# Kernel optimization log

Measured on AMD Instinct MI355X. Metric: run time of the kernel, lower is better.

Reference implementation:

```python
import jax, jax.numpy as jnp
import numpy as np

N = 131072
BETA = 1.0
E = float(np.e)
BISECT_ITERS = 60  # (v-u)/2^60 << 1e-5 threshold of FIND_MIN


def _smooth_l1(x, beta=BETA):
    d = jnp.abs(x)
    return jnp.where(d < beta, 0.5 * d * d / beta, d - 0.5 * beta)


def _safe_log(w):
    return jnp.log(jnp.maximum(w, 1e-12))


def _eps(w, wp, wh, beta=BETA):
    # epsilon(omega) = smooth_l1((omega-omega_hat)/2) + smooth_l1(log omega - log omega_p)
    return _smooth_l1((w - wh) * 0.5, beta) + _smooth_l1(_safe_log(w) - _safe_log(wp), beta)


def _eps_prime(w, wp, wh, beta=BETA):
    x = (w - wh) * 0.5
    diff = _safe_log(w) - _safe_log(wp)
    return 0.5 * jnp.clip(x / beta, -1.0, 1.0) + jnp.clip(diff / beta, -1.0, 1.0) / jnp.maximum(w, 1e-12)


def _sigma(w, wp, wh, beta=BETA):
    return w * _eps_prime(w, wp, wh, beta)


def _find_min(u, v, f):
    # Vectorized FIND_MIN bisection: fixed-trip bisection + boundary cases.
    u0, v0 = u, v

    def body(_, uv):
        uu, vv = uv
        m = (uu + vv) * 0.5
        c = f(m) >= 0
        return (jnp.where(c, uu, m), jnp.where(c, m, vv))

    uf, vf = jax.lax.fori_loop(0, BISECT_ITERS, body, (u, v))
    m = (uf + vf) * 0.5
    return jnp.where(f(u0) >= 0, u0, jnp.where(f(v0) <= 0, v0, m))


def _solve_o1(wp, wh, a1, b1, beta=BETA):
    w0 = b1 - a1
    fm_e = lambda u, v: _find_min(u, v, lambda w: _eps_prime(w, wp, wh, beta))
    fm_s = lambda u, v: _find_min(u, v, lambda w: _sigma(w, wp, wh, beta))
    branchA = jnp.maximum(w0, wh) < wp
    branchB = jnp.maximum(w0, wp) < wh
    cA = fm_e(jnp.maximum(w0, wh), wp)
    ebeta = float(np.exp(beta))
    # J1..J5 intervals from J_getter
    c2 = fm_e(jnp.maximum(w0, wp), jnp.minimum(float(np.exp(min(beta, 1.0))) * wp, wh))
    c3 = fm_e(jnp.maximum(jnp.maximum(w0, 2.0 * float(np.sqrt(beta))), jnp.maximum(wh - 2.0 * beta, ebeta * wp)), wh)
    base = jnp.maximum(w0, jnp.maximum(wh - 2.0 * beta, E * wp))
    c4 = fm_s(base, jnp.minimum(ebeta, wh))
    disc = jnp.sqrt(jnp.maximum(1.0 - 32.0 / jnp.maximum(wh * wh, 1e-12), 0.0))
    c5 = fm_s(base, jnp.minimum(jnp.minimum(ebeta * wp, wh), wh * 0.25 * (1.0 + disc)))
    c6 = fm_s(jnp.maximum(base, wh * 0.25 * (1.0 - disc)), jnp.minimum(ebeta * wp, wh))
    small = wh <= 4.0 * float(np.sqrt(2.0))
    cands = jnp.stack([w0, wh, c2, c3, c4, c5, c6], axis=-1)  # [N,7]
    evals = _eps(cands, wp[..., None], wh[..., None], beta)
    zeros = jnp.zeros_like(small)
    invalid = jnp.stack([zeros, zeros, zeros, zeros, ~small, small, small], axis=-1)
    evals = jnp.where(invalid, jnp.float32(1e30), evals)
    idx = jnp.argmin(evals, axis=-1)
    wB = jnp.take_along_axis(cands, idx[..., None], axis=-1)[..., 0]
    return jnp.where(branchA, cA, jnp.where(branchB, wB, w0))


def _solve_o2(dp, wp, a2, b2, beta=BETA):
    wh1 = 2.0 * (dp - a2)
    wh2 = 2.0 * (b2 - dp)
    trivial = wp >= jnp.maximum(wh1, wh2)
    w1 = _solve_o1(wp, wh1, a2, b2, beta)
    w2 = _solve_o1(wp, wh2, a2, b2, beta)
    pick1 = _eps(w1, wp, wh1, beta) <= _eps(w2, wp, wh2, beta)
    d = jnp.where(pick1, a2 + 0.5 * w1, b2 + 0.5 * w2)
    w = jnp.where(pick1, w1, w2)
    return jnp.where(trivial, dp, d), jnp.where(trivial, wp, w)


def _case_axis(pred, prop, cases, target, crop, axis):
    if axis == 0:
        lt, rb = cases[:, 0], cases[:, 1]
        d_id, o_id = 0, 2
    else:
        lt, rb = cases[:, 2], cases[:, 3]
        d_id, o_id = 1, 3
    pd, po = pred[:, d_id], pred[:, o_id]
    td, to = target[:, d_id], target[:, o_id]
    ca = 0.5 * (prop[:, d_id] + prop[:, o_id])
    da = prop[:, o_id] - prop[:, d_id]
    # right/bottom cut
    a1r = td - 0.5 * to
    b1r = (crop[:, axis] - ca) / da
    wr = _solve_o1(po, 2.0 * (pd - a1r), a1r, b1r)
    dr = a1r + 0.5 * wr
    # left/top cut
    a1l = -ca / da
    b1l = td + 0.5 * to
    wl = _solve_o1(po, 2.0 * (b1l - pd), a1l, b1l)
    dl = b1l - 0.5 * wl
    # both cut (source passes omega_p=pred[:,d_id] and crop[:,d_id] -- replicated)
    b2 = (crop[:, d_id] - ca) / da
    db, wb = _solve_o2(pd, pd, a1l, b2)
    none_c = (~lt) & (~rb)
    r_c = (~lt) & rb
    l_c = lt & (~rb)
    d_lab = jnp.where(none_c, td, jnp.where(r_c, dr, jnp.where(l_c, dl, db)))
    w_lab = jnp.where(none_c, to, jnp.where(r_c, wr, jnp.where(l_c, wl, wb)))
    return d_lab, w_lab


def setup_inputs() -> dict:
    key = jax.random.key(0)
    k = jax.random.split(key, 8)
    img = jax.random.normal(k[0], (1, 3, 128, 128), jnp.float32)
    pred = jax.random.normal(k[1], (N, 4), jnp.float32) * 0.3
    target = jax.random.normal(k[2], (N, 4), jnp.float32) * 0.3
    xy1 = jax.random.uniform(k[3], (N, 2), jnp.float32) * 800.0
    wh = jax.random.uniform(k[4], (N, 2), jnp.float32) * 180.0 + 20.0
    proposal_list = jnp.stack([xy1[:, 0], xy1[:, 1], xy1[:, 0] + wh[:, 0], xy1[:, 1] + wh[:, 1]], axis=1)
    crop_shapes = jax.random.uniform(k[5], (N, 4), jnp.float32) * 200.0 + 900.0
    cases = jax.random.bernoulli(k[6], 0.5, (N, 4))
    return {"img": img, "pred": pred, "target": target, "crop_shapes": crop_shapes,
            "proposal_list": proposal_list, "cases": cases, "sampling_results": 0}


def reference(img, pred, target, crop_shapes, proposal_list, cases, sampling_results):
    # target/pred dw,dh (cols 2,3) are exponentiated to widths/heights, as in forward
    predw = pred.at[:, 2:4].set(jnp.exp(pred[:, 2:4]))
    targw = target.at[:, 2:4].set(jnp.exp(target[:, 2:4]))
    d0, w0 = _case_axis(predw, proposal_list, cases, targw, crop_shapes, 0)
    d1, w1 = _case_axis(predw, proposal_list, cases, targw, crop_shapes, 1)
    # label layout [dx, dy, w, h] matching label[0..3] of the source
    return jnp.stack([d0, d1, w0, w1], axis=-1)
```

## Files before the change

### kernel.cpp

```cpp
#include <hip/hip_runtime.h>
#include <math.h>

#define BISECT_ITERS 60
#define N_ROWS 131072
#define N_PAIRS (2 * N_ROWS)
#define BLOCK 512
#define NW (BLOCK / 64)

#define E_CONST 2.71828182845904523536f
#define SMALL_THRESH 5.65685424949238019520f
#define LN2F 0.69314718055994530942f
#define LOG1EM12 -27.63102111592854820f

__device__ __forceinline__ float log_cr(float wc) {
    double d = (double)wc;
    long long b = __double_as_longlong(d);
    int e = (int)((b >> 52) & 0x7FF) - 1023;
    double m = __longlong_as_double((b & 0x000FFFFFFFFFFFFFLL) |
                                    0x3FF0000000000000LL);
    if (m > 1.3333333333333333) {
        m *= 0.5;
        e += 1;
    }
    double s = (m - 1.0) / (m + 1.0);
    double s2 = s * s;
    double p = 1.0 / 17.0;
    p = fma(p, s2, 1.0 / 15.0);
    p = fma(p, s2, 1.0 / 13.0);
    p = fma(p, s2, 1.0 / 11.0);
    p = fma(p, s2, 1.0 / 9.0);
    p = fma(p, s2, 1.0 / 7.0);
    p = fma(p, s2, 1.0 / 5.0);
    p = fma(p, s2, 1.0 / 3.0);
    p = fma(p, s2, 1.0);
    double res = fma(2.0 * s, p, (double)e * 0.69314718055994530941723212145818);
    return (float)res;
}

__device__ __forceinline__ float safe_log_f(float w) {
    if (w <= 1e-12f) return LOG1EM12;
    return log_cr(w);
}

__device__ __forceinline__ float clip1f(float x) {
#pragma clang fp contract(off)
    return fminf(fmaxf(x, -1.0f), 1.0f);
}

__device__ __forceinline__ float sl1(float x) {
#pragma clang fp contract(off)
    float d = fabsf(x);
    return (d < 1.0f) ? (0.5f * d) * d : d - 0.5f;
}

__device__ __forceinline__ float eps_f(float w, float wh, float lwp) {
#pragma clang fp contract(off)
    return sl1((w - wh) * 0.5f) + sl1(safe_log_f(w) - lwp);
}

__device__ __forceinline__ float eps_prime_cr(float w, float wh, float lwp) {
#pragma clang fp contract(off)
    float x = (w - wh) * 0.5f;
    float diff = safe_log_f(w) - lwp;
    return 0.5f * clip1f(x) + clip1f(diff) / fmaxf(w, 1e-12f);
}

__device__ __forceinline__ float sigma_cr(float w, float wh, float lwp) {
#pragma clang fp contract(off)
    return w * eps_prime_cr(w, wh, lwp);
}

__device__ __forceinline__ float nlogf(float w) {
    return LN2F * __builtin_amdgcn_logf(fmaxf(w, 1e-12f));
}

__device__ __forceinline__ float epsp_sign(float m, float wh, float lwp) {
    float wm = fmaxf(m, 1e-12f);
    float x = (m - wh) * 0.5f;
    float diff = __builtin_fmaf(LN2F, __builtin_amdgcn_logf(wm), -lwp);
    return __builtin_fmaf(0.5f * clip1f(x), wm, clip1f(diff));
}

__device__ __forceinline__ int fast_epsp_sgn(float x, float wh, float lwp) {
    float wm = fmaxf(x, 1e-12f);
    float F = epsp_sign(x, wh, lwp);
    float tau = 2e-5f * (wm + 1.0f);
    if (F > tau) return 1;
    if (F < -tau) return -1;
    return 0;
}

__device__ __forceinline__ int fast_sigma_sgn(float x, float wh, float lwp) {
    float wm = fmaxf(x, 1e-12f);
    float F = epsp_sign(x, wh, lwp);
    float G = x * F;
    float tau = fabsf(x) * (2e-5f * (wm + 1.0f));
    if (G > tau) return 1;
    if (G < -tau) return -1;
    return 0;
}

__device__ __forceinline__ float fast_eval(float w, float wh, float lwp) {
#pragma clang fp contract(off)
    return sl1((w - wh) * 0.5f) + sl1(nlogf(w) - lwp);
}

__device__ float find_min_e(float u, float v, float wh, float lwp) {
#pragma clang fp contract(off)
    float u0 = u, v0 = v;
#pragma unroll 1
    for (int i = 0; i < BISECT_ITERS; ++i) {
        float m = (u + v) * 0.5f;
        bool frozen = (m == u) || (m == v);
        bool c = epsp_sign(m, wh, lwp) >= 0.0f;
        u = c ? u : m;
        v = c ? m : v;
        if (__all(frozen)) break;
    }
    float m = (u + v) * 0.5f;
    float r = m;
    if (eps_prime_cr(v0, wh, lwp) <= 0.0f) r = v0;
    if (eps_prime_cr(u0, wh, lwp) >= 0.0f) r = u0;
    return r;
}

__device__ __forceinline__ bool ov_e_le(float x, float wh, float lwp) {
    int s = fast_epsp_sgn(x, wh, lwp);
    if (s < 0) return true;
    if (s > 0) return false;
    return eps_prime_cr(x, wh, lwp) <= 0.0f;
}
__device__ __forceinline__ bool ov_e_ge(float x, float wh, float lwp) {
    int s = fast_epsp_sgn(x, wh, lwp);
    if (s > 0) return true;
    if (s < 0) return false;
    return eps_prime_cr(x, wh, lwp) >= 0.0f;
}
__device__ __forceinline__ bool ov_s_le(float x, float wh, float lwp) {
    int s = fast_sigma_sgn(x, wh, lwp);
    if (s < 0) return true;
    if (s > 0) return false;
    return sigma_cr(x, wh, lwp) <= 0.0f;
}
__device__ __forceinline__ bool ov_s_ge(float x, float wh, float lwp) {
    int s = fast_sigma_sgn(x, wh, lwp);
    if (s > 0) return true;
    if (s < 0) return false;
    return sigma_cr(x, wh, lwp) >= 0.0f;
}

__device__ __forceinline__ float argmin7(const float* cands, const float* Ef,
                                         const bool* valid, float wh, float lwp) {
#pragma clang fp contract(off)
    int j = 0;
    float best = Ef[0];
#pragma unroll
    for (int k = 1; k < 7; ++k) {
        if (Ef[k] < best) { best = Ef[k]; j = k; }
    }
    bool need_cr = false;
#pragma unroll
    for (int k = 0; k < 7; ++k) {
        if (k == j) continue;
        float dl = 2e-5f + 2e-6f * (fabsf(best) + fabsf(Ef[k]));
        if (Ef[k] < best + dl &&
            fabsf(cands[k] - cands[j]) > 1e-4f * (1.0f + fabsf(cands[j])))
            need_cr = true;
    }
    if (need_cr) {
        float Ec[7];
#pragma unroll
        for (int k = 0; k < 7; ++k)
            Ec[k] = valid[k] ? eps_f(cands[k], wh, lwp) : 1e30f;
        j = 0;
        best = Ec[0];
#pragma unroll
        for (int k = 1; k < 7; ++k) {
            if (Ec[k] < best) { best = Ec[k]; j = k; }
        }
    }
    return cands[j];
}

struct PairP {
    float pd, po, td, to, a1r, b1r, a1l, b1l;
    int lt, rb;
};

__device__ __forceinline__ PairP load_pair(const float* __restrict__ pred,
                                           const float* __restrict__ target,
                                           const float* __restrict__ crop,
                                           const float* __restrict__ prop,
                                           const int* __restrict__ cases,
                                           int pair) {
#pragma clang fp contract(off)
    int row = pair >> 1, axis = pair & 1;
    int d_id = axis, o_id = axis + 2, r4 = row * 4;
    PairP P;
    P.pd = pred[r4 + d_id];
    P.po = (float)exp((double)pred[r4 + o_id]);
    P.td = target[r4 + d_id];
    P.to = (float)exp((double)target[r4 + o_id]);
    float p_d = prop[r4 + d_id];
    float p_o = prop[r4 + o_id];
    float ca = 0.5f * (p_d + p_o);
    float da = p_o - p_d;
    float crop_a = crop[r4 + axis];
    P.a1r = P.td - 0.5f * P.to;
    P.b1r = (crop_a - ca) / da;
    P.a1l = (-ca) / da;
    P.b1l = P.td + 0.5f * P.to;
    P.lt = cases[r4 + 2 * axis];
    P.rb = cases[r4 + 2 * axis + 1];
    return P;
}

__device__ float solve_B_large(float wp, float wh, float w0, float lwp) {
#pragma clang fp contract(off)
    float ewp = E_CONST * wp;
    float base = fmaxf(w0, fmaxf(wh - 2.0f, ewp));
    float disc = sqrtf(fmaxf(1.0f - 32.0f / fmaxf(wh * wh, 1e-12f), 0.0f));

    float u2 = fmaxf(w0, wp), v2 = fminf(ewp, wh);
    float u3 = fmaxf(fmaxf(w0, 2.0f), fmaxf(wh - 2.0f, ewp)), v3 = wh;
    float u5 = base, v5 = fminf(fminf(ewp, wh), (wh * 0.25f) * (1.0f + disc));
    float u6 = fmaxf(base, (wh * 0.25f) * (1.0f - disc)), v6 = fminf(ewp, wh);
    float u02 = u2, v02 = v2, u03 = u3, v03 = v3;
    float u05 = u5, v05 = v5, u06 = u6, v06 = v6;

#pragma unroll 1
    for (int i = 0; i < BISECT_ITERS; ++i) {
        float m2 = (u2 + v2) * 0.5f;
        float m3 = (u3 + v3) * 0.5f;
        float m5 = (u5 + v5) * 0.5f;
        float m6 = (u6 + v6) * 0.5f;
        bool fr = (m2 == u2 || m2 == v2) && (m3 == u3 || m3 == v3) &&
                  (m5 == u5 || m5 == v5) && (m6 == u6 || m6 == v6);
        bool c2 = epsp_sign(m2, wh, lwp) >= 0.0f;
        bool c3 = epsp_sign(m3, wh, lwp) >= 0.0f;
        bool c5 = (m5 * epsp_sign(m5, wh, lwp)) >= 0.0f;
        bool c6 = (m6 * epsp_sign(m6, wh, lwp)) >= 0.0f;
        u2 = c2 ? u2 : m2; v2 = c2 ? m2 : v2;
        u3 = c3 ? u3 : m3; v3 = c3 ? m3 : v3;
        u5 = c5 ? u5 : m5; v5 = c5 ? m5 : v5;
        u6 = c6 ? u6 : m6; v6 = c6 ? m6 : v6;
        if (__all(fr)) break;
    }

    float c2r = (u2 + v2) * 0.5f;
    if (ov_e_le(v02, wh, lwp)) c2r = v02;
    if (ov_e_ge(u02, wh, lwp)) c2r = u02;
    float c3r = (u3 + v3) * 0.5f;
    if (ov_e_le(v03, wh, lwp)) c3r = v03;
    if (ov_e_ge(u03, wh, lwp)) c3r = u03;
    float c5r = (u5 + v5) * 0.5f;
    if (ov_s_le(v05, wh, lwp)) c5r = v05;
    if (ov_s_ge(u05, wh, lwp)) c5r = u05;
    float c6r = (u6 + v6) * 0.5f;
    if (ov_s_le(v06, wh, lwp)) c6r = v06;
    if (ov_s_ge(u06, wh, lwp)) c6r = u06;

    float cands[7] = {w0, wh, c2r, c3r, 0.0f, c5r, c6r};
    bool valid[7] = {true, true, true, true, false, true, true};
    float Ef[7];
    Ef[0] = fast_eval(w0, wh, lwp);
    Ef[1] = fast_eval(wh, wh, lwp);
    Ef[2] = fast_eval(c2r, wh, lwp);
    Ef[3] = fast_eval(c3r, wh, lwp);
    Ef[4] = 1e30f;
    Ef[5] = fast_eval(c5r, wh, lwp);
    Ef[6] = fast_eval(c6r, wh, lwp);
    return argmin7(cands, Ef, valid, wh, lwp);
}

__device__ float solve_B_small(float wp, float wh, float w0, float lwp) {
#pragma clang fp contract(off)
    float ewp = E_CONST * wp;
    float base = fmaxf(w0, fmaxf(wh - 2.0f, ewp));

    float u2 = fmaxf(w0, wp), v2 = fminf(ewp, wh);
    float u3 = fmaxf(fmaxf(w0, 2.0f), fmaxf(wh - 2.0f, ewp)), v3 = wh;
    float u4 = base, v4 = fminf(E_CONST, wh);
    float u02 = u2, v02 = v2, u03 = u3, v03 = v3, u04 = u4, v04 = v4;

#pragma unroll 1
    for (int i = 0; i < BISECT_ITERS; ++i) {
        float m2 = (u2 + v2) * 0.5f;
        float m3 = (u3 + v3) * 0.5f;
        float m4 = (u4 + v4) * 0.5f;
        bool fr = (m2 == u2 || m2 == v2) && (m3 == u3 || m3 == v3) &&
                  (m4 == u4 || m4 == v4);
        bool c2 = epsp_sign(m2, wh, lwp) >= 0.0f;
        bool c3 = epsp_sign(m3, wh, lwp) >= 0.0f;
        bool c4 = (m4 * epsp_sign(m4, wh, lwp)) >= 0.0f;
        u2 = c2 ? u2 : m2; v2 = c2 ? m2 : v2;
        u3 = c3 ? u3 : m3; v3 = c3 ? m3 : v3;
        u4 = c4 ? u4 : m4; v4 = c4 ? m4 : v4;
        if (__all(fr)) break;
    }

    float c2r = (u2 + v2) * 0.5f;
    if (ov_e_le(v02, wh, lwp)) c2r = v02;
    if (ov_e_ge(u02, wh, lwp)) c2r = u02;
    float c3r = (u3 + v3) * 0.5f;
    if (ov_e_le(v03, wh, lwp)) c3r = v03;
    if (ov_e_ge(u03, wh, lwp)) c3r = u03;
    float c4r = (u4 + v4) * 0.5f;
    if (ov_s_le(v04, wh, lwp)) c4r = v04;
    if (ov_s_ge(u04, wh, lwp)) c4r = u04;

    float cands[7] = {w0, wh, c2r, c3r, c4r, 0.0f, 0.0f};
    bool valid[7] = {true, true, true, true, true, false, false};
    float Ef[7];
    Ef[0] = fast_eval(w0, wh, lwp);
    Ef[1] = fast_eval(wh, wh, lwp);
    Ef[2] = fast_eval(c2r, wh, lwp);
    Ef[3] = fast_eval(c3r, wh, lwp);
    Ef[4] = fast_eval(c4r, wh, lwp);
    Ef[5] = 1e30f;
    Ef[6] = 1e30f;
    return argmin7(cands, Ef, valid, wh, lwp);
}

__global__ __launch_bounds__(BLOCK)
void cabb_fused_kernel(const float* __restrict__ pred,
                       const float* __restrict__ target,
                       const float* __restrict__ crop,
                       const float* __restrict__ prop,
                       const int* __restrict__ cases,
                       float* __restrict__ out) {
#pragma clang fp contract(off)
    __shared__ float qb_wp[2 * BLOCK], qb_wh[2 * BLOCK], qb_w0[2 * BLOCK];
    __shared__ unsigned short qb_code[2 * BLOCK];
    __shared__ float qa_wp[BLOCK], qa_wh[BLOCK], qa_w0[BLOCK];
    __shared__ unsigned short qa_code[BLOCK];
    __shared__ float s_res[2 * BLOCK];
    __shared__ int s_cnt[NW][3];
    __shared__ int s_tot[3];

    int tid = threadIdx.x;
    int wid = tid >> 6;
    int lane = tid & 63;
    unsigned long long lower = (1ULL << lane) - 1ULL;
    int pair = blockIdx.x * BLOCK + tid;

    if (tid < 3) s_tot[tid] = 0;

    PairP P = load_pair(pred, target, crop, prop, cases, pair);

    bool need_b = P.lt && P.rb;
    bool need_l = P.lt && !P.rb;
    bool need_r = !P.lt && P.rb;

    int it_type[2] = {-1, -1};
    float it_wp[2], it_wh[2], it_w0[2];
    unsigned short it_code[2];
    int nit = 0;

    if (need_r || need_l) {
        float wp = P.po;
        float wh = need_l ? 2.0f * (P.b1l - P.pd) : 2.0f * (P.pd - P.a1r);
        float w0 = need_l ? (P.b1l - P.a1l) : (P.b1r - P.a1r);
        bool bA = fmaxf(w0, wh) < wp;
        bool bB = fmaxf(w0, wp) < wh;
        if (bA || bB) {
            it_type[0] = bA ? 2 : (wh <= SMALL_THRESH ? 1 : 0);
            it_wp[0] = wp; it_wh[0] = wh; it_w0[0] = w0;
            it_code[0] = (unsigned short)(tid * 2);
            nit = 1;
        }
    } else if (need_b) {
        float wh1 = 2.0f * (P.pd - P.a1l);
        float wh2 = 2.0f * (P.b1r - P.pd);
        bool trivial = P.pd >= fmaxf(wh1, wh2);
        if (!trivial) {
            float w0 = P.b1r - P.a1l;
            for (int s = 0; s < 2; ++s) {
                float wh = s ? wh2 : wh1;
                bool bA = fmaxf(w0, wh) < P.pd;
                bool bB = fmaxf(w0, P.pd) < wh;
                if (bA || bB) {
                    it_type[nit] = bA ? 2 : (wh <= SMALL_THRESH ? 1 : 0);
                    it_wp[nit] = P.pd; it_wh[nit] = wh; it_w0[nit] = w0;
                    it_code[nit] = (unsigned short)(tid * 2 + s);
                    ++nit;
                }
            }
        }
    }

    for (int k = 0; k < 2; ++k) {
        bool is0 = it_type[k] == 0, is1 = it_type[k] == 1, is2 = it_type[k] == 2;
        unsigned long long m0 = __ballot(is0);
        unsigned long long m1 = __ballot(is1);
        unsigned long long m2 = __ballot(is2);
        if (lane == 0) {
            s_cnt[wid][0] = __popcll(m0);
            s_cnt[wid][1] = __popcll(m1);
            s_cnt[wid][2] = __popcll(m2);
        }
        __syncthreads();
        if (it_type[k] >= 0) {
            int t = it_type[k];
            int base = s_tot[t];
            for (int w = 0; w < wid; ++w) base += s_cnt[w][t];
            unsigned long long mm = t == 0 ? m0 : (t == 1 ? m1 : m2);
            int pos = base + __popcll(mm & lower);
            if (t == 0) {
                qb_wp[pos] = it_wp[k]; qb_wh[pos] = it_wh[k];
                qb_w0[pos] = it_w0[k]; qb_code[pos] = it_code[k];
            } else if (t == 1) {
                int p2 = (2 * BLOCK - 1) - pos;
                qb_wp[p2] = it_wp[k]; qb_wh[p2] = it_wh[k];
                qb_w0[p2] = it_w0[k]; qb_code[p2] = it_code[k];
            } else {
                qa_wp[pos] = it_wp[k]; qa_wh[pos] = it_wh[k];
                qa_w0[pos] = it_w0[k]; qa_code[pos] = it_code[k];
            }
        }
        __syncthreads();
        if (tid < 3) {
            int s = 0;
            for (int w = 0; w < NW; ++w) s += s_cnt[w][tid];
            s_tot[tid] += s;
        }
        __syncthreads();
    }

    int nBl = s_tot[0], nBs = s_tot[1], nA = s_tot[2];

    int nBlC = (nBl + 63) >> 6;
    int nBsC = (nBs + 63) >> 6;
    int nAC = (nA + 63) >> 6;
    int totC = nBlC + nBsC + nAC;
    for (int c = wid; c < totC; c += NW) {
        if (c < nBlC) {
            int i = (c << 6) + lane;
            if (i < nBl) {
                float wp = qb_wp[i], wh = qb_wh[i], w0 = qb_w0[i];
                float lwp = safe_log_f(wp);
                s_res[qb_code[i]] = solve_B_large(wp, wh, w0, lwp);
            }
        } else if (c < nBlC + nBsC) {
            int i = ((c - nBlC) << 6) + lane;
            if (i < nBs) {
                int idx = (2 * BLOCK - 1) - i;
                float wp = qb_wp[idx], wh = qb_wh[idx], w0 = qb_w0[idx];
                float lwp = safe_log_f(wp);
                s_res[qb_code[idx]] = solve_B_small(wp, wh, w0, lwp);
            }
        } else {
            int i = ((c - nBlC - nBsC) << 6) + lane;
            if (i < nA) {
                float wp = qa_wp[i], wh = qa_wh[i], w0 = qa_w0[i];
                float lwp = safe_log_f(wp);
                s_res[qa_code[i]] = find_min_e(fmaxf(w0, wh), wp, wh, lwp);
            }
        }
    }
    __syncthreads();

    int row = pair >> 1, axis = pair & 1;
    int r4 = row * 4;
    float d_lab, w_lab;
    if (need_b) {
        float wh1 = 2.0f * (P.pd - P.a1l);
        float wh2 = 2.0f * (P.b1r - P.pd);
        bool trivial = P.pd >= fmaxf(wh1, wh2);
        if (trivial) {
            d_lab = P.pd;
            w_lab = P.pd;
        } else {
            float w0 = P.b1r - P.a1l;
            bool q1 = (fmaxf(w0, wh1) < P.pd) || (fmaxf(w0, P.pd) < wh1);
            bool q2 = (fmaxf(w0, wh2) < P.pd) || (fmaxf(w0, P.pd) < wh2);
            float s1 = q1 ? s_res[tid * 2] : w0;
            float s2 = q2 ? s_res[tid * 2 + 1] : w0;
            float lwpf = nlogf(P.pd);
            float F1 = sl1((s1 - wh1) * 0.5f) + sl1(nlogf(s1) - lwpf);
            float F2 = sl1((s2 - wh2) * 0.5f) + sl1(nlogf(s2) - lwpf);
            float dl = 3e-5f + 2e-6f * (fabsf(F1) + fabsf(F2));
            bool pick1;
            if (F1 <= F2 - dl) {
                pick1 = true;
            } else if (F1 > F2 + dl) {
                pick1 = false;
            } else {
                float lwp = safe_log_f(P.pd);
                pick1 = eps_f(s1, wh1, lwp) <= eps_f(s2, wh2, lwp);
            }
            d_lab = pick1 ? (P.a1l + 0.5f * s1) : (P.b1r + 0.5f * s2);
            w_lab = pick1 ? s1 : s2;
        }
    } else if (need_l) {
        float wh = 2.0f * (P.b1l - P.pd);
        float w0 = P.b1l - P.a1l;
        bool q = (fmaxf(w0, wh) < P.po) || (fmaxf(w0, P.po) < wh);
        float s = q ? s_res[tid * 2] : w0;
        d_lab = P.b1l - 0.5f * s;
        w_lab = s;
    } else if (need_r) {
        float wh = 2.0f * (P.pd - P.a1r);
        float w0 = P.b1r - P.a1r;
        bool q = (fmaxf(w0, wh) < P.po) || (fmaxf(w0, P.po) < wh);
        float s = q ? s_res[tid * 2] : w0;
        d_lab = P.a1r + 0.5f * s;
        w_lab = s;
    } else {
        d_lab = P.td;
        w_lab = P.to;
    }

    out[r4 + axis] = d_lab;
    out[r4 + 2 + axis] = w_lab;
}

extern "C" void kernel_launch(void* const* d_in, const int* in_sizes, int n_in,
                              void* d_out, int out_size, void* d_ws, size_t ws_size,
                              hipStream_t stream) {
    const float* pred = (const float*)d_in[1];
    const float* target = (const float*)d_in[2];
    const float* crop = (const float*)d_in[3];
    const float* prop = (const float*)d_in[4];
    const int* cases = (const int*)d_in[5];
    float* out = (float*)d_out;

    cabb_fused_kernel<<<N_PAIRS / BLOCK, BLOCK, 0, stream>>>(
        pred, target, crop, prop, cases, out);
}
```

Before: 86.25 us.

## Unify bisection solvers into one branch-free routine with a single work queue

Merges the large-B, small-B and A-branch solvers into one routine that always runs four bisections, masking unused ones with degenerate intervals. The three per-type queues become one compacted queue, which cuts ballot/scan rounds and barriers and lets every wavefront run the same code. It also adds an early-exit test that stops bisection once the interval falls below a relative 1e-5 width. The cost is extra wasted lanes on A and small-B items, plus possible result differences from the looser convergence test.

```diff
diff --git a/kernel.cpp b/kernel.cpp
--- a/kernel.cpp
+++ b/kernel.cpp
@@ -105,25 +105,6 @@
     return sl1((w - wh) * 0.5f) + sl1(nlogf(w) - lwp);
 }
 
-__device__ float find_min_e(float u, float v, float wh, float lwp) {
-#pragma clang fp contract(off)
-    float u0 = u, v0 = v;
-#pragma unroll 1
-    for (int i = 0; i < BISECT_ITERS; ++i) {
-        float m = (u + v) * 0.5f;
-        bool frozen = (m == u) || (m == v);
-        bool c = epsp_sign(m, wh, lwp) >= 0.0f;
-        u = c ? u : m;
-        v = c ? m : v;
-        if (__all(frozen)) break;
-    }
-    float m = (u + v) * 0.5f;
-    float r = m;
-    if (eps_prime_cr(v0, wh, lwp) <= 0.0f) r = v0;
-    if (eps_prime_cr(u0, wh, lwp) >= 0.0f) r = u0;
-    return r;
-}
-
 __device__ __forceinline__ bool ov_e_le(float x, float wh, float lwp) {
     int s = fast_epsp_sgn(x, wh, lwp);
     if (s < 0) return true;
@@ -180,6 +161,11 @@
         }
     }
     return cands[j];
+}
+
+__device__ __forceinline__ bool cvg(float u, float v, float m) {
+    return (m == u) || (m == v) ||
+           (fabsf(v - u) <= 1e-5f * fmaxf(1.0f, fabsf(m)));
 }
 
 struct PairP {
@@ -215,111 +201,70 @@
     return P;
 }
 
-__device__ float solve_B_large(float wp, float wh, float w0, float lwp) {
-#pragma clang fp contract(off)
+__device__ float solve_unified(int type, float wp, float wh, float w0, float lwp) {
+#pragma clang fp contract(off)
+    bool isA = (type == 2);
+    bool small_ = (type == 1);
     float ewp = E_CONST * wp;
     float base = fmaxf(w0, fmaxf(wh - 2.0f, ewp));
     float disc = sqrtf(fmaxf(1.0f - 32.0f / fmaxf(wh * wh, 1e-12f), 0.0f));
 
-    float u2 = fmaxf(w0, wp), v2 = fminf(ewp, wh);
-    float u3 = fmaxf(fmaxf(w0, 2.0f), fmaxf(wh - 2.0f, ewp)), v3 = wh;
-    float u5 = base, v5 = fminf(fminf(ewp, wh), (wh * 0.25f) * (1.0f + disc));
-    float u6 = fmaxf(base, (wh * 0.25f) * (1.0f - disc)), v6 = fminf(ewp, wh);
+    float u2 = isA ? fmaxf(w0, wh) : fmaxf(w0, wp);
+    float v2 = isA ? wp : fminf(ewp, wh);
+    float u3 = fmaxf(fmaxf(w0, 2.0f), fmaxf(wh - 2.0f, ewp));
+    float v3 = isA ? u3 : wh;
+    float u4 = base;
+    float v4 = isA ? base
+                   : (small_ ? fminf(E_CONST, wh)
+                             : fminf(fminf(ewp, wh),
+                                     (wh * 0.25f) * (1.0f + disc)));
+    float u6 = fmaxf(base, (wh * 0.25f) * (1.0f - disc));
+    float v6 = (isA || small_) ? u6 : fminf(ewp, wh);
+
     float u02 = u2, v02 = v2, u03 = u3, v03 = v3;
-    float u05 = u5, v05 = v5, u06 = u6, v06 = v6;
-
-#pragma unroll 1
-    for (int i = 0; i < BISECT_ITERS; ++i) {
-        float m2 = (u2 + v2) * 0.5f;
-        float m3 = (u3 + v3) * 0.5f;
-        float m5 = (u5 + v5) * 0.5f;
-        float m6 = (u6 + v6) * 0.5f;
-        bool fr = (m2 == u2 || m2 == v2) && (m3 == u3 || m3 == v3) &&
-                  (m5 == u5 || m5 == v5) && (m6 == u6 || m6 == v6);
-        bool c2 = epsp_sign(m2, wh, lwp) >= 0.0f;
-        bool c3 = epsp_sign(m3, wh, lwp) >= 0.0f;
-        bool c5 = (m5 * epsp_sign(m5, wh, lwp)) >= 0.0f;
-        bool c6 = (m6 * epsp_sign(m6, wh, lwp)) >= 0.0f;
-        u2 = c2 ? u2 : m2; v2 = c2 ? m2 : v2;
-        u3 = c3 ? u3 : m3; v3 = c3 ? m3 : v3;
-        u5 = c5 ? u5 : m5; v5 = c5 ? m5 : v5;
-        u6 = c6 ? u6 : m6; v6 = c6 ? m6 : v6;
-        if (__all(fr)) break;
-    }
-
-    float c2r = (u2 + v2) * 0.5f;
-    if (ov_e_le(v02, wh, lwp)) c2r = v02;
-    if (ov_e_ge(u02, wh, lwp)) c2r = u02;
-    float c3r = (u3 + v3) * 0.5f;
-    if (ov_e_le(v03, wh, lwp)) c3r = v03;
-    if (ov_e_ge(u03, wh, lwp)) c3r = u03;
-    float c5r = (u5 + v5) * 0.5f;
-    if (ov_s_le(v05, wh, lwp)) c5r = v05;
-    if (ov_s_ge(u05, wh, lwp)) c5r = u05;
-    float c6r = (u6 + v6) * 0.5f;
-    if (ov_s_le(v06, wh, lwp)) c6r = v06;
-    if (ov_s_ge(u06, wh, lwp)) c6r = u06;
-
-    float cands[7] = {w0, wh, c2r, c3r, 0.0f, c5r, c6r};
-    bool valid[7] = {true, true, true, true, false, true, true};
-    float Ef[7];
-    Ef[0] = fast_eval(w0, wh, lwp);
-    Ef[1] = fast_eval(wh, wh, lwp);
-    Ef[2] = fast_eval(c2r, wh, lwp);
-    Ef[3] = fast_eval(c3r, wh, lwp);
-    Ef[4] = 1e30f;
-    Ef[5] = fast_eval(c5r, wh, lwp);
-    Ef[6] = fast_eval(c6r, wh, lwp);
-    return argmin7(cands, Ef, valid, wh, lwp);
-}
-
-__device__ float solve_B_small(float wp, float wh, float w0, float lwp) {
-#pragma clang fp contract(off)
-    float ewp = E_CONST * wp;
-    float base = fmaxf(w0, fmaxf(wh - 2.0f, ewp));
-
-    float u2 = fmaxf(w0, wp), v2 = fminf(ewp, wh);
-    float u3 = fmaxf(fmaxf(w0, 2.0f), fmaxf(wh - 2.0f, ewp)), v3 = wh;
-    float u4 = base, v4 = fminf(E_CONST, wh);
-    float u02 = u2, v02 = v2, u03 = u3, v03 = v3, u04 = u4, v04 = v4;
+    float u04 = u4, v04 = v4, u06 = u6, v06 = v6;
 
 #pragma unroll 1
     for (int i = 0; i < BISECT_ITERS; ++i) {
         float m2 = (u2 + v2) * 0.5f;
         float m3 = (u3 + v3) * 0.5f;
         float m4 = (u4 + v4) * 0.5f;
-        bool fr = (m2 == u2 || m2 == v2) && (m3 == u3 || m3 == v3) &&
-                  (m4 == u4 || m4 == v4);
+        float m6 = (u6 + v6) * 0.5f;
+        bool fr = cvg(u2, v2, m2) && cvg(u3, v3, m3) &&
+                  cvg(u4, v4, m4) && cvg(u6, v6, m6);
         bool c2 = epsp_sign(m2, wh, lwp) >= 0.0f;
         bool c3 = epsp_sign(m3, wh, lwp) >= 0.0f;
         bool c4 = (m4 * epsp_sign(m4, wh, lwp)) >= 0.0f;
+        bool c6 = (m6 * epsp_sign(m6, wh, lwp)) >= 0.0f;
         u2 = c2 ? u2 : m2; v2 = c2 ? m2 : v2;
         u3 = c3 ? u3 : m3; v3 = c3 ? m3 : v3;
         u4 = c4 ? u4 : m4; v4 = c4 ? m4 : v4;
+        u6 = c6 ? u6 : m6; v6 = c6 ? m6 : v6;
         if (__all(fr)) break;
     }
 
-    float c2r = (u2 + v2) * 0.5f;
-    if (ov_e_le(v02, wh, lwp)) c2r = v02;
-    if (ov_e_ge(u02, wh, lwp)) c2r = u02;
-    float c3r = (u3 + v3) * 0.5f;
-    if (ov_e_le(v03, wh, lwp)) c3r = v03;
-    if (ov_e_ge(u03, wh, lwp)) c3r = u03;
-    float c4r = (u4 + v4) * 0.5f;
-    if (ov_s_le(v04, wh, lwp)) c4r = v04;
-    if (ov_s_ge(u04, wh, lwp)) c4r = u04;
-
-    float cands[7] = {w0, wh, c2r, c3r, c4r, 0.0f, 0.0f};
-    bool valid[7] = {true, true, true, true, true, false, false};
+    float r2 = (u2 + v2) * 0.5f;
+    if (ov_e_le(v02, wh, lwp)) r2 = v02;
+    if (ov_e_ge(u02, wh, lwp)) r2 = u02;
+    float r3 = (u3 + v3) * 0.5f;
+    if (ov_e_le(v03, wh, lwp)) r3 = v03;
+    if (ov_e_ge(u03, wh, lwp)) r3 = u03;
+    float r4 = (u4 + v4) * 0.5f;
+    if (ov_s_le(v04, wh, lwp)) r4 = v04;
+    if (ov_s_ge(u04, wh, lwp)) r4 = u04;
+    float r6 = (u6 + v6) * 0.5f;
+    if (ov_s_le(v06, wh, lwp)) r6 = v06;
+    if (ov_s_ge(u06, wh, lwp)) r6 = u06;
+
+    float cands[7] = {w0, wh, r2, r3, r4, r4, r6};
+    bool valid[7] = {!isA, !isA, !isA, !isA,
+                     small_, !isA && !small_, !isA && !small_};
     float Ef[7];
-    Ef[0] = fast_eval(w0, wh, lwp);
-    Ef[1] = fast_eval(wh, wh, lwp);
-    Ef[2] = fast_eval(c2r, wh, lwp);
-    Ef[3] = fast_eval(c3r, wh, lwp);
-    Ef[4] = fast_eval(c4r, wh, lwp);
-    Ef[5] = 1e30f;
-    Ef[6] = 1e30f;
-    return argmin7(cands, Ef, valid, wh, lwp);
+#pragma unroll
+    for (int k = 0; k < 7; ++k)
+        Ef[k] = valid[k] ? fast_eval(cands[k], wh, lwp) : 1e30f;
+    float wB = argmin7(cands, Ef, valid, wh, lwp);
+    return isA ? r2 : wB;
 }
 
 __global__ __launch_bounds__(BLOCK)
@@ -330,21 +275,16 @@
                        const int* __restrict__ cases,
                        float* __restrict__ out) {
 #pragma clang fp contract(off)
-    __shared__ float qb_wp[2 * BLOCK], qb_wh[2 * BLOCK], qb_w0[2 * BLOCK];
-    __shared__ unsigned short qb_code[2 * BLOCK];
-    __shared__ float qa_wp[BLOCK], qa_wh[BLOCK], qa_w0[BLOCK];
-    __shared__ unsigned short qa_code[BLOCK];
+    __shared__ float q_wp[2 * BLOCK], q_wh[2 * BLOCK], q_w0[2 * BLOCK];
+    __shared__ unsigned short q_code[2 * BLOCK];
     __shared__ float s_res[2 * BLOCK];
-    __shared__ int s_cnt[NW][3];
-    __shared__ int s_tot[3];
+    __shared__ int s_cnt[NW];
 
     int tid = threadIdx.x;
     int wid = tid >> 6;
     int lane = tid & 63;
     unsigned long long lower = (1ULL << lane) - 1ULL;
     int pair = blockIdx.x * BLOCK + tid;
-
-    if (tid < 3) s_tot[tid] = 0;
 
     PairP P = load_pair(pred, target, crop, prop, cases, pair);
 
@@ -389,73 +329,40 @@
         }
     }
 
-    for (int k = 0; k < 2; ++k) {
-        bool is0 = it_type[k] == 0, is1 = it_type[k] == 1, is2 = it_type[k] == 2;
-        unsigned long long m0 = __ballot(is0);
-        unsigned long long m1 = __ballot(is1);
-        unsigned long long m2 = __ballot(is2);
-        if (lane == 0) {
-            s_cnt[wid][0] = __popcll(m0);
-            s_cnt[wid][1] = __popcll(m1);
-            s_cnt[wid][2] = __popcll(m2);
-        }
-        __syncthreads();
-        if (it_type[k] >= 0) {
-            int t = it_type[k];
-            int base = s_tot[t];
-            for (int w = 0; w < wid; ++w) base += s_cnt[w][t];
-            unsigned long long mm = t == 0 ? m0 : (t == 1 ? m1 : m2);
-            int pos = base + __popcll(mm & lower);
-            if (t == 0) {
-                qb_wp[pos] = it_wp[k]; qb_wh[pos] = it_wh[k];
-                qb_w0[pos] = it_w0[k]; qb_code[pos] = it_code[k];
-            } else if (t == 1) {
-                int p2 = (2 * BLOCK - 1) - pos;
-                qb_wp[p2] = it_wp[k]; qb_wh[p2] = it_wh[k];
-                qb_w0[p2] = it_w0[k]; qb_code[p2] = it_code[k];
-            } else {
-                qa_wp[pos] = it_wp[k]; qa_wh[pos] = it_wh[k];
-                qa_w0[pos] = it_w0[k]; qa_code[pos] = it_code[k];
-            }
-        }
-        __syncthreads();
-        if (tid < 3) {
-            int s = 0;
-            for (int w = 0; w < NW; ++w) s += s_cnt[w][tid];
-            s_tot[tid] += s;
-        }
-        __syncthreads();
-    }
-
-    int nBl = s_tot[0], nBs = s_tot[1], nA = s_tot[2];
-
-    int nBlC = (nBl + 63) >> 6;
-    int nBsC = (nBs + 63) >> 6;
-    int nAC = (nA + 63) >> 6;
-    int totC = nBlC + nBsC + nAC;
-    for (int c = wid; c < totC; c += NW) {
-        if (c < nBlC) {
-            int i = (c << 6) + lane;
-            if (i < nBl) {
-                float wp = qb_wp[i], wh = qb_wh[i], w0 = qb_w0[i];
-                float lwp = safe_log_f(wp);
-                s_res[qb_code[i]] = solve_B_large(wp, wh, w0, lwp);
-            }
-        } else if (c < nBlC + nBsC) {
-            int i = ((c - nBlC) << 6) + lane;
-            if (i < nBs) {
-                int idx = (2 * BLOCK - 1) - i;
-                float wp = qb_wp[idx], wh = qb_wh[idx], w0 = qb_w0[idx];
-                float lwp = safe_log_f(wp);
-                s_res[qb_code[idx]] = solve_B_small(wp, wh, w0, lwp);
-            }
-        } else {
-            int i = ((c - nBlC - nBsC) << 6) + lane;
-            if (i < nA) {
-                float wp = qa_wp[i], wh = qa_wh[i], w0 = qa_w0[i];
-                float lwp = safe_log_f(wp);
-                s_res[qa_code[i]] = find_min_e(fmaxf(w0, wh), wp, wh, lwp);
-            }
+    bool h0 = it_type[0] >= 0;
+    bool h1 = it_type[1] >= 0;
+    unsigned long long mA = __ballot(h0);
+    unsigned long long mB = __ballot(h1);
+    int popA = __popcll(mA);
+    if (lane == 0) s_cnt[wid] = popA + __popcll(mB);
+    __syncthreads();
+    int qbase = 0, nQ = 0;
+#pragma unroll
+    for (int w = 0; w < NW; ++w) {
+        int c = s_cnt[w];
+        if (w < wid) qbase += c;
+        nQ += c;
+    }
+    if (h0) {
+        int p = qbase + __popcll(mA & lower);
+        q_wp[p] = it_wp[0]; q_wh[p] = it_wh[0]; q_w0[p] = it_w0[0];
+        q_code[p] = (unsigned short)(it_code[0] | (it_type[0] << 12));
+    }
+    if (h1) {
+        int p = qbase + popA + __popcll(mB & lower);
+        q_wp[p] = it_wp[1]; q_wh[p] = it_wh[1]; q_w0[p] = it_w0[1];
+        q_code[p] = (unsigned short)(it_code[1] | (it_type[1] << 12));
+    }
+    __syncthreads();
+
+    int chunks = (nQ + 63) >> 6;
+    for (int c = wid; c < chunks; c += NW) {
+        int i = (c << 6) + lane;
+        if (i < nQ) {
+            float wp = q_wp[i], wh = q_wh[i], w0 = q_w0[i];
+            int cc = q_code[i];
+            float lwp = safe_log_f(wp);
+            s_res[cc & 0xFFF] = solve_unified(cc >> 12, wp, wh, w0, lwp);
         }
     }
     __syncthreads();
```

After: 85.28 us. About the same (-1.1%).
